# Optimization experiments

Measured on AMD Instinct MI355X. Metric: run time of the kernel, lower is better.

Reference implementation:

```python
import jax, jax.numpy as jnp
import numpy as np

N, D = 2048, 1024
H, KV, HD = 16, 4, 64
REPEATS = H // KV
SCALE = HD ** -0.5


def setup_inputs() -> dict:
    key = jax.random.key(0)
    ks = jax.random.split(key, 6)
    x = jax.random.normal(ks[0], (N, D), dtype=jnp.float32)
    # rotary tables: cos/sin of interleaved-pair angles (llama-style view_as_complex)
    pos = jnp.arange(N, dtype=jnp.float32)[:, None]
    inv_freq = 1.0 / (10000.0 ** (jnp.arange(0, HD, 2, dtype=jnp.float32) / HD))
    ang = pos * inv_freq[None, :]  # (N, HD//2)
    freqs_cos = jnp.cos(ang)
    freqs_sin = jnp.sin(ang)
    s = 0.02
    Wq = jax.random.normal(ks[1], (D, H * HD), dtype=jnp.float32) * s
    Wk = jax.random.normal(ks[2], (D, KV * HD), dtype=jnp.float32) * s
    Wv = jax.random.normal(ks[3], (D, KV * HD), dtype=jnp.float32) * s
    Wo = jax.random.normal(ks[4], (H * HD, D), dtype=jnp.float32) * s
    return {"x": x, "freqs_cos": freqs_cos, "freqs_sin": freqs_sin,
            "Wq": Wq, "Wk": Wk, "Wv": Wv, "Wo": Wo}


def _rope(t, cos, sin):
    # t: (N, heads, HD); interleaved complex pairs (even=real, odd=imag)
    tr = t[..., 0::2]
    ti = t[..., 1::2]
    c = cos[:, None, :]
    s = sin[:, None, :]
    out_r = tr * c - ti * s
    out_i = tr * s + ti * c
    return jnp.stack([out_r, out_i], axis=-1).reshape(t.shape)


def reference(x, freqs_cos, freqs_sin, Wq, Wk, Wv, Wo):
    n = x.shape[0]
    xq = (x @ Wq).reshape(n, H, HD)
    xk = (x @ Wk).reshape(n, KV, HD)
    xv = (x @ Wv).reshape(n, KV, HD)
    xq = _rope(xq, freqs_cos, freqs_sin)
    xk = _rope(xk, freqs_cos, freqs_sin)
    # repeat_kv along head dim (GQA)
    k = jnp.repeat(xk, REPEATS, axis=1)  # (n, H, HD)
    v = jnp.repeat(xv, REPEATS, axis=1)
    # memory_efficient_attention with mask=None: full attention over token axis
    scores = jnp.einsum('nhd,mhd->hnm', xq, k) * SCALE
    attn = jax.nn.softmax(scores, axis=-1)
    out = jnp.einsum('hnm,mhd->nhd', attn, v)
    return out.reshape(n, H * HD) @ Wo
```

## Files before the change

### kernel.cpp

```cpp
#include <hip/hip_runtime.h>

#define N_TOK 2048
#define DMODEL 1024
#define NH 16
#define NKV 4
#define HDIM 64
#define SCALE_LOG2E 0.1803368801111204f

typedef __attribute__((ext_vector_type(8))) short short8;
typedef __attribute__((ext_vector_type(4))) float f32x4;
typedef __attribute__((ext_vector_type(16))) float f32x16;
typedef __attribute__((ext_vector_type(2))) int i32x2;
typedef __attribute__((ext_vector_type(4))) unsigned int u32x4;
typedef unsigned short u16;
typedef unsigned int u32;

__device__ __forceinline__ u16 f2bf(float x) {
    u32 u = __float_as_uint(x);
    u += 0x7FFF + ((u >> 16) & 1);
    return (u16)(u >> 16);
}
__device__ __forceinline__ u32 pack2(float a, float b) {
    return (u32)f2bf(a) | ((u32)f2bf(b) << 16);
}
__device__ __forceinline__ u32 pack2t(float a, float b) {
    return __builtin_amdgcn_perm(__float_as_uint(b), __float_as_uint(a), 0x07060302u);
}

__device__ __forceinline__ void gload16(const u16* g, u16* l) {
    __builtin_amdgcn_global_load_lds(
        (const __attribute__((address_space(1))) unsigned int*)g,
        (__attribute__((address_space(3))) unsigned int*)l, 16, 0, 0);
}

__global__ __launch_bounds__(256) void prep(
    const float* __restrict__ Wq, const float* __restrict__ Wk,
    const float* __restrict__ Wv, const float* __restrict__ Wo,
    const float* __restrict__ x,
    u16* __restrict__ Wqt, u16* __restrict__ Wkt, u16* __restrict__ Wvt,
    u16* __restrict__ Wot, u16* __restrict__ xb)
{
    const int z = blockIdx.z;
    const int t = threadIdx.x;
    if (z == 4) {
        size_t base = ((size_t)(blockIdx.y * 16 + blockIdx.x)) * 8192;
#pragma unroll
        for (int i = 0; i < 8; ++i) {
            float4 v = *(const float4*)(x + base + i * 1024 + t * 4);
            uint2 p; p.x = pack2(v.x, v.y); p.y = pack2(v.z, v.w);
            *(uint2*)(xb + base + i * 1024 + t * 4) = p;
        }
        return;
    }
    const float* W; u16* Wt; int NC;
    if      (z == 0) { W = Wq; Wt = Wqt; NC = 1024; }
    else if (z == 1) { W = Wk; Wt = Wkt; NC = 256; }
    else if (z == 2) { W = Wv; Wt = Wvt; NC = 256; }
    else             { W = Wo; Wt = Wot; NC = 1024; }
    const int n0 = blockIdx.x * 64;
    if (n0 >= NC) return;
    const int k0 = blockIdx.y * 64;
    __shared__ float T[64][68];
    const int row = t >> 2, cs = (t & 3) * 16;
#pragma unroll
    for (int i = 0; i < 4; ++i)
        *(float4*)&T[row][cs + i * 4] =
            *(const float4*)(W + (size_t)(k0 + row) * NC + n0 + cs + i * 4);
    __syncthreads();
    const int nl = t >> 2, ks = (t & 3) * 16;
    u32 pk[8];
#pragma unroll
    for (int i = 0; i < 8; ++i)
        pk[i] = pack2(T[ks + 2 * i][nl], T[ks + 2 * i + 1][nl]);
    u16* dst = Wt + (size_t)(n0 + nl) * DMODEL + k0 + ks;
    uint4 w0; w0.x = pk[0]; w0.y = pk[1]; w0.z = pk[2]; w0.w = pk[3];
    uint4 w1; w1.x = pk[4]; w1.y = pk[5]; w1.z = pk[6]; w1.w = pk[7];
    *(uint4*)(dst) = w0;
    *(uint4*)(dst + 8) = w1;
}

__global__ __launch_bounds__(256, 3) void gemm_qkv(
    const u16* __restrict__ A,
    const u16* __restrict__ B0, const u16* __restrict__ B1, const u16* __restrict__ B2,
    u16* __restrict__ D0, u16* __restrict__ FKout, u16* __restrict__ FVout,
    const float* __restrict__ fc, const float* __restrict__ fs)
{
    __shared__ u16 As[3][64][64];
    __shared__ u16 Bs[3][64][64];
    const int t = threadIdx.x;
    const int m0 = blockIdx.x * 64;
    const int by = blockIdx.y;

    const u16* Bt; int nl0, ep;
    float epsc = 1.f;
    if (by < 16)      { Bt = B0; nl0 = by * 64;        ep = 1; epsc = SCALE_LOG2E; }
    else if (by < 20) { Bt = B1; nl0 = (by - 16) * 64; ep = 3; }
    else              { Bt = B2; nl0 = (by - 20) * 64; ep = 2; }

    const int w = t >> 6, lane = t & 63;
    const int quad = lane >> 4, l15 = lane & 15;
    const int wm = (w >> 1) * 32, wn = (w & 1) * 32;
    const int rx = l15 & 7;

    const int sro = w * 16 + (lane >> 3);
    const int sco = ((lane & 7) ^ (lane >> 3)) * 8;
    const u16* ApL = A + (size_t)(m0 + sro) * DMODEL + sco;
    const u16* BpL = Bt + (size_t)(nl0 + sro) * DMODEL + sco;

    f32x4 acc[2][2];
#pragma unroll
    for (int i = 0; i < 2; ++i)
#pragma unroll
        for (int j = 0; j < 2; ++j) acc[i][j] = {0.f, 0.f, 0.f, 0.f};

#pragma unroll
    for (int k = 0; k < 2; ++k) {
        gload16(ApL + k * 8 * DMODEL, &As[0][w * 16 + k * 8][0]);
        gload16(BpL + k * 8 * DMODEL, &Bs[0][w * 16 + k * 8][0]);
    }
#pragma unroll
    for (int k = 0; k < 2; ++k) {
        gload16(ApL + k * 8 * DMODEL + 64, &As[1][w * 16 + k * 8][0]);
        gload16(BpL + k * 8 * DMODEL + 64, &Bs[1][w * 16 + k * 8][0]);
    }
    asm volatile("s_waitcnt vmcnt(4)" ::: "memory");
    __builtin_amdgcn_sched_barrier(0);
    __builtin_amdgcn_s_barrier();

    int cb = 0, nb = 1, pb = 2;
    for (int it = 0; it < 16; ++it) {
        if (it + 2 < 16) {
            const int kk = (it + 2) * 64;
#pragma unroll
            for (int k = 0; k < 2; ++k) {
                gload16(ApL + k * 8 * DMODEL + kk, &As[pb][w * 16 + k * 8][0]);
                gload16(BpL + k * 8 * DMODEL + kk, &Bs[pb][w * 16 + k * 8][0]);
            }
        }
#pragma unroll
        for (int c = 0; c < 2; ++c) {
            short8 af[2], bf[2];
#pragma unroll
            for (int i = 0; i < 2; ++i)
                af[i] = *(const short8*)&As[cb][wm + i * 16 + l15][((4 * c + quad) ^ rx) * 8];
#pragma unroll
            for (int j = 0; j < 2; ++j)
                bf[j] = *(const short8*)&Bs[cb][wn + j * 16 + l15][((4 * c + quad) ^ rx) * 8];
#pragma unroll
            for (int i = 0; i < 2; ++i)
#pragma unroll
                for (int j = 0; j < 2; ++j)
                    acc[i][j] = __builtin_amdgcn_mfma_f32_16x16x32_bf16(af[i], bf[j], acc[i][j], 0, 0, 0);
        }
        if (it + 2 < 16) asm volatile("s_waitcnt vmcnt(4)" ::: "memory");
        else             asm volatile("s_waitcnt vmcnt(0)" ::: "memory");
        __builtin_amdgcn_sched_barrier(0);
        __builtin_amdgcn_s_barrier();
        const int tmp = cb; cb = nb; nb = pb; pb = tmp;
    }

#pragma unroll
    for (int i = 0; i < 2; ++i)
#pragma unroll
        for (int j = 0; j < 2; ++j) {
            const int cl = nl0 + wn + j * 16 + l15;
            if (ep == 1) {
#pragma unroll
                for (int r4 = 0; r4 < 4; ++r4) {
                    const int r = m0 + wm + i * 16 + quad * 4 + r4;
                    float own = acc[i][j][r4];
                    float other = __shfl_xor(own, 1, 64);
                    const int p = (cl & 63) >> 1;
                    const float c = fc[r * 32 + p] * epsc, s = fs[r * 32 + p] * epsc;
                    float outv = ((cl & 1) == 0) ? (own * c - other * s)
                                                 : (other * s + own * c);
                    D0[(size_t)r * 1024 + cl] = f2bf(outv);
                }
            } else if (ep == 3) {
#pragma unroll
                for (int r4 = 0; r4 < 4; ++r4) {
                    const int r = m0 + wm + i * 16 + quad * 4 + r4;
                    float own = acc[i][j][r4];
                    float other = __shfl_xor(own, 1, 64);
                    const int p = (cl & 63) >> 1;
                    const float c = fc[r * 32 + p], s = fs[r * 32 + p];
                    float outv = ((cl & 1) == 0) ? (own * c - other * s)
                                                 : (other * s + own * c);
                    const int kvh2 = cl >> 6, d = cl & 63;
                    const int s2 = d >> 4, hi2 = (d >> 3) & 1, jv = d & 7;
                    const int kh2 = r >> 10, rd2 = (r >> 6) & 15;
                    const int kg2 = (r >> 5) & 1, l31v = r & 31;
                    size_t idx = ((((((size_t)(kvh2 * 2 + kh2) * 16 + rd2) * 2 + kg2)
                                    * 4 + s2) * 2 + hi2) * 32 + l31v) * 8 + jv;
                    FKout[idx] = f2bf(outv);
                }
            } else {
                const int rb = m0 + wm + i * 16 + quad * 4;
                const int g = cl >> 6, d = cl & 63;
                const int d2 = d >> 5, dl = d & 31;
                const int keyblk = rb >> 7, kg = (rb >> 5) & 3;
                const int kst = (rb >> 4) & 1, hb = (rb >> 3) & 1, jv = rb & 7;
                size_t idx = ((((((size_t)(g * 16 + keyblk) * 4 + kg) * 2 + kst) * 2 + d2)
                               * 2 + hb) * 32 + dl) * 8 + jv;
                uint2 pk;
                pk.x = pack2(acc[i][j][0], acc[i][j][1]);
                pk.y = pack2(acc[i][j][2], acc[i][j][3]);
                *(uint2*)(FVout + idx) = pk;
            }
        }
}

__global__ __launch_bounds__(256, 2) void gemm_out(
    const u16* __restrict__ A, const u16* __restrict__ Bt, float* __restrict__ Dout)
{
    __shared__ u16 As[3][64][64];
    __shared__ u16 Bs[3][64][64];
    const int t = threadIdx.x;
    const int m0 = blockIdx.x * 64;
    const int nl0 = blockIdx.y * 64;

    const int w = t >> 6, lane = t & 63;
    const int quad = lane >> 4, l15 = lane & 15;
    const int wm = (w >> 1) * 32, wn = (w & 1) * 32;
    const int rx = l15 & 7;

    const int sro = w * 16 + (lane >> 3);
    const int sco = ((lane & 7) ^ (lane >> 3)) * 8;
    const u16* ApL = A + (size_t)(m0 + sro) * DMODEL + sco;
    const u16* BpL = Bt + (size_t)(nl0 + sro) * DMODEL + sco;

    f32x4 acc[2][2];
#pragma unroll
    for (int i = 0; i < 2; ++i)
#pragma unroll
        for (int j = 0; j < 2; ++j) acc[i][j] = {0.f, 0.f, 0.f, 0.f};

#pragma unroll
    for (int k = 0; k < 2; ++k) {
        gload16(ApL + k * 8 * DMODEL, &As[0][w * 16 + k * 8][0]);
        gload16(BpL + k * 8 * DMODEL, &Bs[0][w * 16 + k * 8][0]);
    }
#pragma unroll
    for (int k = 0; k < 2; ++k) {
        gload16(ApL + k * 8 * DMODEL + 64, &As[1][w * 16 + k * 8][0]);
        gload16(BpL + k * 8 * DMODEL + 64, &Bs[1][w * 16 + k * 8][0]);
    }
    asm volatile("s_waitcnt vmcnt(4)" ::: "memory");
    __builtin_amdgcn_sched_barrier(0);
    __builtin_amdgcn_s_barrier();

    int cb = 0, nb = 1, pb = 2;
    for (int it = 0; it < 16; ++it) {
        if (it + 2 < 16) {
            const int kk = (it + 2) * 64;
#pragma unroll
            for (int k = 0; k < 2; ++k) {
                gload16(ApL + k * 8 * DMODEL + kk, &As[pb][w * 16 + k * 8][0]);
                gload16(BpL + k * 8 * DMODEL + kk, &Bs[pb][w * 16 + k * 8][0]);
            }
        }
#pragma unroll
        for (int c = 0; c < 2; ++c) {
            short8 af[2], bf[2];
#pragma unroll
            for (int i = 0; i < 2; ++i)
                af[i] = *(const short8*)&As[cb][wm + i * 16 + l15][((4 * c + quad) ^ rx) * 8];
#pragma unroll
            for (int j = 0; j < 2; ++j)
                bf[j] = *(const short8*)&Bs[cb][wn + j * 16 + l15][((4 * c + quad) ^ rx) * 8];
#pragma unroll
            for (int i = 0; i < 2; ++i)
#pragma unroll
                for (int j = 0; j < 2; ++j)
                    acc[i][j] = __builtin_amdgcn_mfma_f32_16x16x32_bf16(af[i], bf[j], acc[i][j], 0, 0, 0);
        }
        if (it + 2 < 16) asm volatile("s_waitcnt vmcnt(4)" ::: "memory");
        else             asm volatile("s_waitcnt vmcnt(0)" ::: "memory");
        __builtin_amdgcn_sched_barrier(0);
        __builtin_amdgcn_s_barrier();
        const int tmp = cb; cb = nb; nb = pb; pb = tmp;
    }

#pragma unroll
    for (int i = 0; i < 2; ++i)
#pragma unroll
        for (int j = 0; j < 2; ++j) {
            const int cl = nl0 + wn + j * 16 + l15;
#pragma unroll
            for (int r4 = 0; r4 < 4; ++r4) {
                const int r = m0 + wm + i * 16 + quad * 4 + r4;
                Dout[(size_t)r * 1024 + cl] = acc[i][j][r4];
            }
        }
}

__global__ __launch_bounds__(256, 2) void attn(
    const u16* __restrict__ Qb, const u16* __restrict__ FK,
    const u16* __restrict__ FV, u16* __restrict__ Ob)
{
    __shared__ float Xf[4160];

    const int t = threadIdx.x;
    const int n0 = blockIdx.x * 64;
    const int h = blockIdx.y, kvh = h >> 2;
    const int w = t >> 6, lane = t & 63;
    const int hi = lane >> 5, l31 = lane & 31;
    const int qgrp = w & 1, khalf = w >> 1;

    const short8 ones = {(short)0x3F80, (short)0x3F80, (short)0x3F80, (short)0x3F80,
                         (short)0x3F80, (short)0x3F80, (short)0x3F80, (short)0x3F80};

    const u16* qp = Qb + (size_t)(n0 + qgrp * 32 + l31) * (NH * HDIM) + h * HDIM + hi * 8;
    short8 qf[4];
#pragma unroll
    for (int s = 0; s < 4; ++s) qf[s] = *(const short8*)(qp + s * 16);

    const u16* fkb = FK + ((size_t)(kvh * 2 + khalf)) * 65536 + (size_t)lane * 8;
    const u16* fvb = FV + ((size_t)kvh) * 131072 + (size_t)lane * 8;

    f32x16 o[2], o_l;
#pragma unroll
    for (int d2 = 0; d2 < 2; ++d2)
#pragma unroll
        for (int r = 0; r < 16; ++r) o[d2][r] = 0.f;
#pragma unroll
    for (int r = 0; r < 16; ++r) o_l[r] = 0.f;

    short8 kfa[4], kfb2[4];
#pragma unroll
    for (int s = 0; s < 4; ++s) kfa[s]  = *(const short8*)(fkb + s * 512);
#pragma unroll
    for (int s = 0; s < 4; ++s) kfb2[s] = *(const short8*)(fkb + 2048 + s * 512);

    for (int rd = 0; rd < 16; ++rd) {
        const int rdn = (rd + 1) & 15;

        short8 vf[2][2][2];
#pragma unroll
        for (int kg = 0; kg < 2; ++kg) {
            const int kg_global = khalf * 32 + rd * 2 + kg;
            const int keyblk = kg_global >> 2, kgi = kg_global & 3;
#pragma unroll
            for (int s = 0; s < 2; ++s)
#pragma unroll
                for (int d2 = 0; d2 < 2; ++d2)
                    vf[kg][s][d2] = *(const short8*)(fvb +
                        ((((size_t)keyblk * 4 + kgi) * 2 + s) * 2 + d2) * 512);
        }

        f32x16 sa;
#pragma unroll
        for (int r = 0; r < 16; ++r) sa[r] = 0.f;
        __builtin_amdgcn_s_setprio(1);
#pragma unroll
        for (int s = 0; s < 4; ++s)
            sa = __builtin_amdgcn_mfma_f32_32x32x16_bf16(kfa[s], qf[s], sa, 0, 0, 0);
        __builtin_amdgcn_s_setprio(0);
#pragma unroll
        for (int s = 0; s < 4; ++s)
            kfa[s] = *(const short8*)(fkb + (size_t)rdn * 4096 + s * 512);
        {
            float p[16];
#pragma unroll
            for (int r = 0; r < 16; ++r) p[r] = __builtin_amdgcn_exp2f(sa[r]);
            const u32 A0 = pack2t(p[0],  p[1]),  B0 = pack2t(p[2],  p[3]);
            const u32 C0 = pack2t(p[4],  p[5]),  D0 = pack2t(p[6],  p[7]);
            const u32 E0 = pack2t(p[8],  p[9]),  F0 = pack2t(p[10], p[11]);
            const u32 G0 = pack2t(p[12], p[13]), H0 = pack2t(p[14], p[15]);
            i32x2 X = __builtin_amdgcn_permlane32_swap((int)A0, (int)C0, false, false);
            i32x2 Y = __builtin_amdgcn_permlane32_swap((int)B0, (int)D0, false, false);
            i32x2 Z = __builtin_amdgcn_permlane32_swap((int)E0, (int)G0, false, false);
            i32x2 U = __builtin_amdgcn_permlane32_swap((int)F0, (int)H0, false, false);
            u32x4 t0 = {(u32)X.x, (u32)Y.x, (u32)X.y, (u32)Y.y};
            u32x4 t1 = {(u32)Z.x, (u32)U.x, (u32)Z.y, (u32)U.y};
            const short8 ap0 = __builtin_bit_cast(short8, t0);
            const short8 ap1 = __builtin_bit_cast(short8, t1);
            __builtin_amdgcn_s_setprio(1);
#pragma unroll
            for (int d2 = 0; d2 < 2; ++d2) {
                o[d2] = __builtin_amdgcn_mfma_f32_32x32x16_bf16(ap0, vf[0][0][d2], o[d2], 0, 0, 0);
                o[d2] = __builtin_amdgcn_mfma_f32_32x32x16_bf16(ap1, vf[0][1][d2], o[d2], 0, 0, 0);
            }
            o_l = __builtin_amdgcn_mfma_f32_32x32x16_bf16(ap0, ones, o_l, 0, 0, 0);
            o_l = __builtin_amdgcn_mfma_f32_32x32x16_bf16(ap1, ones, o_l, 0, 0, 0);
            __builtin_amdgcn_s_setprio(0);
        }

#pragma unroll
        for (int r = 0; r < 16; ++r) sa[r] = 0.f;
        __builtin_amdgcn_s_setprio(1);
#pragma unroll
        for (int s = 0; s < 4; ++s)
            sa = __builtin_amdgcn_mfma_f32_32x32x16_bf16(kfb2[s], qf[s], sa, 0, 0, 0);
        __builtin_amdgcn_s_setprio(0);
#pragma unroll
        for (int s = 0; s < 4; ++s)
            kfb2[s] = *(const short8*)(fkb + (size_t)rdn * 4096 + 2048 + s * 512);
        {
            float p[16];
#pragma unroll
            for (int r = 0; r < 16; ++r) p[r] = __builtin_amdgcn_exp2f(sa[r]);
            const u32 A0 = pack2t(p[0],  p[1]),  B0 = pack2t(p[2],  p[3]);
            const u32 C0 = pack2t(p[4],  p[5]),  D0 = pack2t(p[6],  p[7]);
            const u32 E0 = pack2t(p[8],  p[9]),  F0 = pack2t(p[10], p[11]);
            const u32 G0 = pack2t(p[12], p[13]), H0 = pack2t(p[14], p[15]);
            i32x2 X = __builtin_amdgcn_permlane32_swap((int)A0, (int)C0, false, false);
            i32x2 Y = __builtin_amdgcn_permlane32_swap((int)B0, (int)D0, false, false);
            i32x2 Z = __builtin_amdgcn_permlane32_swap((int)E0, (int)G0, false, false);
            i32x2 U = __builtin_amdgcn_permlane32_swap((int)F0, (int)H0, false, false);
            u32x4 t0 = {(u32)X.x, (u32)Y.x, (u32)X.y, (u32)Y.y};
            u32x4 t1 = {(u32)Z.x, (u32)U.x, (u32)Z.y, (u32)U.y};
            const short8 ap0 = __builtin_bit_cast(short8, t0);
            const short8 ap1 = __builtin_bit_cast(short8, t1);
            __builtin_amdgcn_s_setprio(1);
#pragma unroll
            for (int d2 = 0; d2 < 2; ++d2) {
                o[d2] = __builtin_amdgcn_mfma_f32_32x32x16_bf16(ap0, vf[1][0][d2], o[d2], 0, 0, 0);
                o[d2] = __builtin_amdgcn_mfma_f32_32x32x16_bf16(ap1, vf[1][1][d2], o[d2], 0, 0, 0);
            }
            o_l = __builtin_amdgcn_mfma_f32_32x32x16_bf16(ap0, ones, o_l, 0, 0, 0);
            o_l = __builtin_amdgcn_mfma_f32_32x32x16_bf16(ap1, ones, o_l, 0, 0, 0);
            __builtin_amdgcn_s_setprio(0);
        }
    }

    if (khalf == 1) {
#pragma unroll
        for (int d2 = 0; d2 < 2; ++d2)
#pragma unroll
            for (int r = 0; r < 16; ++r) {
                const int q32 = (r & 3) + 8 * (r >> 2) + 4 * hi;
                Xf[qgrp * 2048 + q32 * 64 + d2 * 32 + l31] = o[d2][r];
            }
        if (l31 == 0) {
#pragma unroll
            for (int r = 0; r < 16; ++r) {
                const int q32 = (r & 3) + 8 * (r >> 2) + 4 * hi;
                Xf[4096 + qgrp * 32 + q32] = o_l[r];
            }
        }
    }
    __syncthreads();
    if (khalf == 0) {
        float linv[16];
#pragma unroll
        for (int r = 0; r < 16; ++r) {
            const int q32 = (r & 3) + 8 * (r >> 2) + 4 * hi;
            linv[r] = 1.f / (o_l[r] + Xf[4096 + qgrp * 32 + q32]);
        }
#pragma unroll
        for (int d2 = 0; d2 < 2; ++d2)
#pragma unroll
            for (int r = 0; r < 16; ++r) {
                const int q32 = (r & 3) + 8 * (r >> 2) + 4 * hi;
                const float val = o[d2][r] + Xf[qgrp * 2048 + q32 * 64 + d2 * 32 + l31];
                const int qrow = n0 + qgrp * 32 + q32;
                Ob[(size_t)qrow * (NH * HDIM) + h * HDIM + d2 * 32 + l31] = f2bf(val * linv[r]);
            }
    }
}

extern "C" void kernel_launch(void* const* d_in, const int* in_sizes, int n_in,
                              void* d_out, int out_size, void* d_ws, size_t ws_size,
                              hipStream_t stream) {
    const float* x  = (const float*)d_in[0];
    const float* fc = (const float*)d_in[1];
    const float* fs = (const float*)d_in[2];
    const float* Wq = (const float*)d_in[3];
    const float* Wk = (const float*)d_in[4];
    const float* Wv = (const float*)d_in[5];
    const float* Wo = (const float*)d_in[6];
    float* out = (float*)d_out;

    u16* ws  = (u16*)d_ws;
    u16* xb  = ws;
    u16* Wqt = xb  + (size_t)2048 * 1024;
    u16* Wkt = Wqt + (size_t)1024 * 1024;
    u16* Wvt = Wkt + (size_t)256 * 1024;
    u16* Wot = Wvt + (size_t)256 * 1024;
    u16* qb  = Wot + (size_t)1024 * 1024;
    u16* fk  = qb  + (size_t)2048 * 1024;
    u16* fv  = fk  + (size_t)2048 * 256;
    u16* aob = fv  + (size_t)256 * 2048;

    prep<<<dim3(16, 16, 5), dim3(256), 0, stream>>>(Wq, Wk, Wv, Wo, x,
                                                    Wqt, Wkt, Wvt, Wot, xb);
    gemm_qkv<<<dim3(32, 24), dim3(256), 0, stream>>>(xb, Wqt, Wkt, Wvt,
                                                     qb, fk, fv, fc, fs);
    attn<<<dim3(32, 16), dim3(256), 0, stream>>>(qb, fk, fv, aob);
    gemm_out<<<dim3(32, 16), dim3(256), 0, stream>>>(aob, Wot, out);
}
```

Measured before the change: 126.4 us.

## Pre-swizzle QKV GEMM operands into MFMA fragment layout and drop LDS staging

The prep kernel now writes x and Wq/Wk/Wv in bf16 directly in a per-16x32 MFMA fragment order, so each lane's short8 operand is one contiguous 16-byte chunk. gemm_qkv then loads fragments straight from global memory into registers with a two-stage software prefetch, removing LDS tiles, barriers and the async global-to-LDS pipeline. The trade is no data sharing between waves through LDS: each wave refetches its A/B fragments from L2, which raises global load traffic, and register double-buffering depends on latency hiding through occupancy.

```diff
diff --git a/kernel.cpp b/kernel.cpp
--- a/kernel.cpp
+++ b/kernel.cpp
@@ -27,52 +27,91 @@
     return __builtin_amdgcn_perm(__float_as_uint(b), __float_as_uint(a), 0x07060302u);
 }
 
-__device__ __forceinline__ void gload16(const u16* g, u16* l) {
-    __builtin_amdgcn_global_load_lds(
-        (const __attribute__((address_space(1))) unsigned int*)g,
-        (__attribute__((address_space(3))) unsigned int*)l, 16, 0, 0);
-}
-
 __global__ __launch_bounds__(256) void prep(
     const float* __restrict__ Wq, const float* __restrict__ Wk,
     const float* __restrict__ Wv, const float* __restrict__ Wo,
     const float* __restrict__ x,
-    u16* __restrict__ Wqt, u16* __restrict__ Wkt, u16* __restrict__ Wvt,
-    u16* __restrict__ Wot, u16* __restrict__ xb)
+    u16* __restrict__ FBq, u16* __restrict__ FBk, u16* __restrict__ FBv,
+    u16* __restrict__ Wot, u16* __restrict__ FA)
 {
     const int z = blockIdx.z;
     const int t = threadIdx.x;
+    __shared__ float T[64][68];
+
     if (z == 4) {
-        size_t base = ((size_t)(blockIdx.y * 16 + blockIdx.x)) * 8192;
-#pragma unroll
-        for (int i = 0; i < 8; ++i) {
-            float4 v = *(const float4*)(x + base + i * 1024 + t * 4);
-            uint2 p; p.x = pack2(v.x, v.y); p.y = pack2(v.z, v.w);
-            *(uint2*)(xb + base + i * 1024 + t * 4) = p;
-        }
+        const int mt = blockIdx.x, it = blockIdx.y;
+        const int row = t >> 2, cs = (t & 3) * 16;
+#pragma unroll
+        for (int i = 0; i < 4; ++i)
+            *(float4*)&T[row][cs + i * 4] =
+                *(const float4*)(x + (size_t)(mt * 64 + row) * DMODEL + it * 64 + cs + i * 4);
+        __syncthreads();
+        const int ch = t >> 5, tsub = t & 31;
+        const int cc = ch >> 2, mm = ch & 3;
+        const int kl = cc * 32 + (tsub >> 3) * 8;
+        const int ml0 = mm * 16 + (tsub & 7) * 2;
+        u32 pk[8];
+#pragma unroll
+        for (int o = 0; o < 4; ++o)
+            pk[o] = pack2(T[ml0][kl + 2 * o], T[ml0][kl + 2 * o + 1]);
+#pragma unroll
+        for (int o = 0; o < 4; ++o)
+            pk[4 + o] = pack2(T[ml0 + 1][kl + 2 * o], T[ml0 + 1][kl + 2 * o + 1]);
+        u16* dst = FA + (((size_t)(mt * 16 + it) * 2 + cc) * 4 + mm) * 512 + tsub * 16;
+        uint4 w0; w0.x = pk[0]; w0.y = pk[1]; w0.z = pk[2]; w0.w = pk[3];
+        uint4 w1; w1.x = pk[4]; w1.y = pk[5]; w1.z = pk[6]; w1.w = pk[7];
+        *(uint4*)(dst) = w0;
+        *(uint4*)(dst + 8) = w1;
         return;
     }
-    const float* W; u16* Wt; int NC;
-    if      (z == 0) { W = Wq; Wt = Wqt; NC = 1024; }
-    else if (z == 1) { W = Wk; Wt = Wkt; NC = 256; }
-    else if (z == 2) { W = Wv; Wt = Wvt; NC = 256; }
-    else             { W = Wo; Wt = Wot; NC = 1024; }
-    const int n0 = blockIdx.x * 64;
-    if (n0 >= NC) return;
-    const int k0 = blockIdx.y * 64;
-    __shared__ float T[64][68];
+
+    if (z == 3) {
+        const int n0 = blockIdx.x * 64;
+        if (n0 >= 1024) return;
+        const int k0 = blockIdx.y * 64;
+        const int row = t >> 2, cs = (t & 3) * 16;
+#pragma unroll
+        for (int i = 0; i < 4; ++i)
+            *(float4*)&T[row][cs + i * 4] =
+                *(const float4*)(Wo + (size_t)(k0 + row) * 1024 + n0 + cs + i * 4);
+        __syncthreads();
+        const int nl = t >> 2, ks = (t & 3) * 16;
+        u32 pk[8];
+#pragma unroll
+        for (int i = 0; i < 8; ++i)
+            pk[i] = pack2(T[ks + 2 * i][nl], T[ks + 2 * i + 1][nl]);
+        u16* dst = Wot + (size_t)(n0 + nl) * DMODEL + k0 + ks;
+        uint4 w0; w0.x = pk[0]; w0.y = pk[1]; w0.z = pk[2]; w0.w = pk[3];
+        uint4 w1; w1.x = pk[4]; w1.y = pk[5]; w1.z = pk[6]; w1.w = pk[7];
+        *(uint4*)(dst) = w0;
+        *(uint4*)(dst + 8) = w1;
+        return;
+    }
+
+    const float* W; u16* FB; int NC;
+    if      (z == 0) { W = Wq; FB = FBq; NC = 1024; }
+    else if (z == 1) { W = Wk; FB = FBk; NC = 256; }
+    else             { W = Wv; FB = FBv; NC = 256; }
+    const int nt = blockIdx.x, it = blockIdx.y;
+    if (nt * 64 >= NC) return;
     const int row = t >> 2, cs = (t & 3) * 16;
 #pragma unroll
     for (int i = 0; i < 4; ++i)
         *(float4*)&T[row][cs + i * 4] =
-            *(const float4*)(W + (size_t)(k0 + row) * NC + n0 + cs + i * 4);
+            *(const float4*)(W + (size_t)(it * 64 + row) * NC + nt * 64 + cs + i * 4);
     __syncthreads();
-    const int nl = t >> 2, ks = (t & 3) * 16;
+    const int ch = t >> 5, tsub = t & 31;
+    const int cc = ch >> 2, nn = ch & 3;
+    const int kl = cc * 32 + (tsub >> 3) * 8;
+    const int nl0 = nn * 16 + (tsub & 7) * 2;
     u32 pk[8];
 #pragma unroll
-    for (int i = 0; i < 8; ++i)
-        pk[i] = pack2(T[ks + 2 * i][nl], T[ks + 2 * i + 1][nl]);
-    u16* dst = Wt + (size_t)(n0 + nl) * DMODEL + k0 + ks;
+    for (int o = 0; o < 4; ++o)
+        pk[o] = pack2(T[kl + 2 * o][nl0], T[kl + 2 * o + 1][nl0]);
+#pragma unroll
+    for (int o = 0; o < 4; ++o)
+        pk[4 + o] = pack2(T[kl + 2 * o][nl0 + 1], T[kl + 2 * o + 1][nl0 + 1]);
+    u16* dst = FB + (((size_t)(nt * 16 + it) * 2 + cc) * 4 + nn) * 512 + tsub * 16;
     uint4 w0; w0.x = pk[0]; w0.y = pk[1]; w0.z = pk[2]; w0.w = pk[3];
     uint4 w1; w1.x = pk[4]; w1.y = pk[5]; w1.z = pk[6]; w1.w = pk[7];
     *(uint4*)(dst) = w0;
@@ -80,32 +119,30 @@
 }
 
 __global__ __launch_bounds__(256, 3) void gemm_qkv(
-    const u16* __restrict__ A,
-    const u16* __restrict__ B0, const u16* __restrict__ B1, const u16* __restrict__ B2,
+    const u16* __restrict__ FA,
+    const u16* __restrict__ FBq, const u16* __restrict__ FBk, const u16* __restrict__ FBv,
     u16* __restrict__ D0, u16* __restrict__ FKout, u16* __restrict__ FVout,
     const float* __restrict__ fc, const float* __restrict__ fs)
 {
-    __shared__ u16 As[3][64][64];
-    __shared__ u16 Bs[3][64][64];
     const int t = threadIdx.x;
-    const int m0 = blockIdx.x * 64;
+    const int mt = blockIdx.x;
     const int by = blockIdx.y;
-
-    const u16* Bt; int nl0, ep;
+    const int m0 = mt * 64;
+
+    const u16* FB; int nt, nl0, ep;
     float epsc = 1.f;
-    if (by < 16)      { Bt = B0; nl0 = by * 64;        ep = 1; epsc = SCALE_LOG2E; }
-    else if (by < 20) { Bt = B1; nl0 = (by - 16) * 64; ep = 3; }
-    else              { Bt = B2; nl0 = (by - 20) * 64; ep = 2; }
+    if (by < 16)      { FB = FBq; nt = by;      nl0 = by * 64;        ep = 1;
+                        epsc = SCALE_LOG2E; }
+    else if (by < 20) { FB = FBk; nt = by - 16; nl0 = (by - 16) * 64; ep = 3; }
+    else              { FB = FBv; nt = by - 20; nl0 = (by - 20) * 64; ep = 2; }
 
     const int w = t >> 6, lane = t & 63;
     const int quad = lane >> 4, l15 = lane & 15;
     const int wm = (w >> 1) * 32, wn = (w & 1) * 32;
-    const int rx = l15 & 7;
-
-    const int sro = w * 16 + (lane >> 3);
-    const int sco = ((lane & 7) ^ (lane >> 3)) * 8;
-    const u16* ApL = A + (size_t)(m0 + sro) * DMODEL + sco;
-    const u16* BpL = Bt + (size_t)(nl0 + sro) * DMODEL + sco;
+    const int m16b = (w >> 1) * 2, n16b = (w & 1) * 2;
+
+    const u16* fa = FA + (size_t)mt * 65536 + (size_t)m16b * 512 + (size_t)lane * 8;
+    const u16* fb = FB + (size_t)nt * 65536 + (size_t)n16b * 512 + (size_t)lane * 8;
 
     f32x4 acc[2][2];
 #pragma unroll
@@ -113,50 +150,39 @@
 #pragma unroll
         for (int j = 0; j < 2; ++j) acc[i][j] = {0.f, 0.f, 0.f, 0.f};
 
-#pragma unroll
-    for (int k = 0; k < 2; ++k) {
-        gload16(ApL + k * 8 * DMODEL, &As[0][w * 16 + k * 8][0]);
-        gload16(BpL + k * 8 * DMODEL, &Bs[0][w * 16 + k * 8][0]);
-    }
-#pragma unroll
-    for (int k = 0; k < 2; ++k) {
-        gload16(ApL + k * 8 * DMODEL + 64, &As[1][w * 16 + k * 8][0]);
-        gload16(BpL + k * 8 * DMODEL + 64, &Bs[1][w * 16 + k * 8][0]);
-    }
-    asm volatile("s_waitcnt vmcnt(4)" ::: "memory");
-    __builtin_amdgcn_sched_barrier(0);
-    __builtin_amdgcn_s_barrier();
-
-    int cb = 0, nb = 1, pb = 2;
-    for (int it = 0; it < 16; ++it) {
-        if (it + 2 < 16) {
-            const int kk = (it + 2) * 64;
-#pragma unroll
-            for (int k = 0; k < 2; ++k) {
-                gload16(ApL + k * 8 * DMODEL + kk, &As[pb][w * 16 + k * 8][0]);
-                gload16(BpL + k * 8 * DMODEL + kk, &Bs[pb][w * 16 + k * 8][0]);
-            }
-        }
-#pragma unroll
-        for (int c = 0; c < 2; ++c) {
-            short8 af[2], bf[2];
+    short8 a0[2], b0[2], a1[2], b1[2];
+#pragma unroll
+    for (int i = 0; i < 2; ++i) a0[i] = *(const short8*)(fa + i * 512);
+#pragma unroll
+    for (int j = 0; j < 2; ++j) b0[j] = *(const short8*)(fb + j * 512);
+
+    for (int st = 0; st < 32; st += 2) {
+        if (st + 1 < 32) {
+            const int off = (st + 1) * 2048;
+#pragma unroll
+            for (int i = 0; i < 2; ++i) a1[i] = *(const short8*)(fa + off + i * 512);
+#pragma unroll
+            for (int j = 0; j < 2; ++j) b1[j] = *(const short8*)(fb + off + j * 512);
+        }
+#pragma unroll
+        for (int i = 0; i < 2; ++i)
+#pragma unroll
+            for (int j = 0; j < 2; ++j)
+                acc[i][j] = __builtin_amdgcn_mfma_f32_16x16x32_bf16(a0[i], b0[j], acc[i][j], 0, 0, 0);
+        if (st + 2 < 32) {
+            const int off = (st + 2) * 2048;
+#pragma unroll
+            for (int i = 0; i < 2; ++i) a0[i] = *(const short8*)(fa + off + i * 512);
+#pragma unroll
+            for (int j = 0; j < 2; ++j) b0[j] = *(const short8*)(fb + off + j * 512);
+        }
+        if (st + 1 < 32) {
 #pragma unroll
             for (int i = 0; i < 2; ++i)
-                af[i] = *(const short8*)&As[cb][wm + i * 16 + l15][((4 * c + quad) ^ rx) * 8];
-#pragma unroll
-            for (int j = 0; j < 2; ++j)
-                bf[j] = *(const short8*)&Bs[cb][wn + j * 16 + l15][((4 * c + quad) ^ rx) * 8];
-#pragma unroll
-            for (int i = 0; i < 2; ++i)
 #pragma unroll
                 for (int j = 0; j < 2; ++j)
-                    acc[i][j] = __builtin_amdgcn_mfma_f32_16x16x32_bf16(af[i], bf[j], acc[i][j], 0, 0, 0);
-        }
-        if (it + 2 < 16) asm volatile("s_waitcnt vmcnt(4)" ::: "memory");
-        else             asm volatile("s_waitcnt vmcnt(0)" ::: "memory");
-        __builtin_amdgcn_sched_barrier(0);
-        __builtin_amdgcn_s_barrier();
-        const int tmp = cb; cb = nb; nb = pb; pb = tmp;
+                    acc[i][j] = __builtin_amdgcn_mfma_f32_16x16x32_bf16(a1[i], b1[j], acc[i][j], 0, 0, 0);
+        }
     }
 
 #pragma unroll
@@ -210,6 +236,12 @@
         }
 }
 
+__device__ __forceinline__ void gload16(const u16* g, u16* l) {
+    __builtin_amdgcn_global_load_lds(
+        (const __attribute__((address_space(1))) unsigned int*)g,
+        (__attribute__((address_space(3))) unsigned int*)l, 16, 0, 0);
+}
+
 __global__ __launch_bounds__(256, 2) void gemm_out(
     const u16* __restrict__ A, const u16* __restrict__ Bt, float* __restrict__ Dout)
 {
@@ -473,20 +505,20 @@
     float* out = (float*)d_out;
 
     u16* ws  = (u16*)d_ws;
-    u16* xb  = ws;
-    u16* Wqt = xb  + (size_t)2048 * 1024;
-    u16* Wkt = Wqt + (size_t)1024 * 1024;
-    u16* Wvt = Wkt + (size_t)256 * 1024;
-    u16* Wot = Wvt + (size_t)256 * 1024;
-    u16* qb  = Wot + (size_t)1024 * 1024;
+    u16* fa  = ws;
+    u16* fbq = fa  + (size_t)2048 * 1024;
+    u16* fbk = fbq + (size_t)1024 * 1024;
+    u16* fbv = fbk + (size_t)256 * 1024;
+    u16* wot = fbv + (size_t)256 * 1024;
+    u16* qb  = wot + (size_t)1024 * 1024;
     u16* fk  = qb  + (size_t)2048 * 1024;
     u16* fv  = fk  + (size_t)2048 * 256;
     u16* aob = fv  + (size_t)256 * 2048;
 
-    prep<<<dim3(16, 16, 5), dim3(256), 0, stream>>>(Wq, Wk, Wv, Wo, x,
-                                                    Wqt, Wkt, Wvt, Wot, xb);
-    gemm_qkv<<<dim3(32, 24), dim3(256), 0, stream>>>(xb, Wqt, Wkt, Wvt,
+    prep<<<dim3(32, 16, 5), dim3(256), 0, stream>>>(Wq, Wk, Wv, Wo, x,
+                                                    fbq, fbk, fbv, wot, fa);
+    gemm_qkv<<<dim3(32, 24), dim3(256), 0, stream>>>(fa, fbq, fbk, fbv,
                                                      qb, fk, fv, fc, fs);
     attn<<<dim3(32, 16), dim3(256), 0, stream>>>(qb, fk, fv, aob);
-    gemm_out<<<dim3(32, 16), dim3(256), 0, stream>>>(aob, Wot, out);
-}
+    gemm_out<<<dim3(32, 16), dim3(256), 0, stream>>>(aob, wot, out);
+}
```

Result: slower. 135.2 us (+6.9%).
